# Performance work log

Hardware: AMD Instinct MI355X
Metric: run time of the kernel (lower is better)

The kernel has to match this reference:

```python
import jax, jax.numpy as jnp
import numpy as np

B, L, IN_DIM, H, KD = 2, 2048, 1024, 16, 64
SCALE = float(np.sqrt(IN_DIM / H))  # sqrt(in_dim / num_heads), per ScaledDotAttention
LN_EPS = 1e-5


def setup_inputs() -> dict:
    key = jax.random.key(0)
    ks = jax.random.split(key, 12)
    s_in = 1.0 / np.sqrt(IN_DIM)
    s_hd = 1.0 / np.sqrt(H * KD)
    return {
        "q": jax.random.normal(ks[0], (B, L, IN_DIM), jnp.float32),
        "k": jax.random.normal(ks[1], (B, L, IN_DIM), jnp.float32),
        "v": jax.random.normal(ks[2], (B, L, IN_DIM), jnp.float32),
        "Wq": jax.random.normal(ks[3], (IN_DIM, H * KD), jnp.float32) * s_in,
        "bq": jnp.zeros((H * KD,), jnp.float32),
        "Wk": jax.random.normal(ks[4], (IN_DIM, H * KD), jnp.float32) * s_in,
        "bk": jnp.zeros((H * KD,), jnp.float32),
        "Wv": jax.random.normal(ks[5], (IN_DIM, H * KD), jnp.float32) * s_in,
        "bv": jnp.zeros((H * KD,), jnp.float32),
        "Wo": jax.random.normal(ks[6], (H * KD, IN_DIM), jnp.float32) * s_hd,
        "bo": jnp.zeros((IN_DIM,), jnp.float32),
        "gamma": jnp.ones((IN_DIM,), jnp.float32),
        "beta": jnp.zeros((IN_DIM,), jnp.float32),
    }


def _split_heads(x):
    # [B, L, H*KD] -> [H*B, L, KD]  (heads MAJOR, matching permute(2,0,1,3).view)
    b, l, _ = x.shape
    return x.reshape(b, l, H, KD).transpose(2, 0, 1, 3).reshape(H * b, l, KD)


def reference(q, k, v, Wq, bq, Wk, bk, Wv, bv, Wo, bo, gamma, beta):
    res = q
    qh = _split_heads(q @ Wq + bq)   # [H*B, Lq, KD]
    kh = _split_heads(k @ Wk + bk)
    vh = _split_heads(v @ Wv + bv)
    scores = jnp.einsum("zqd,zkd->zqk", qh, kh) / SCALE
    atn = jax.nn.softmax(scores, axis=-1)          # [H*B, Lq, Lk]
    out = jnp.einsum("zqk,zkd->zqd", atn, vh)      # [H*B, Lq, KD]
    b = q.shape[0]
    out = out.reshape(H, b, -1, KD).transpose(1, 2, 0, 3).reshape(b, -1, H * KD)
    out = out @ Wo + bo
    x = out + res
    mu = jnp.mean(x, axis=-1, keepdims=True)
    var = jnp.mean(jnp.square(x - mu), axis=-1, keepdims=True)
    out = (x - mu) * jax.lax.rsqrt(var + LN_EPS) * gamma + beta
    return (out, atn)
```

## Files before the change

kernel.cpp:

```cpp
#include <hip/hip_runtime.h>
#include <hip/hip_bf16.h>

typedef unsigned short u16;
typedef unsigned int   u32;

using bf16x8 = __attribute__((ext_vector_type(8))) short;
using f32x4  = __attribute__((ext_vector_type(4))) float;

#define SEQ  2048
#define NZ   32
#define KTOT 1024
#define NTOT 1024
#define SC2  0.18033688011112042f

__device__ __forceinline__ u16 f2bf(float f) {
    union { float f; u32 u; } x; x.f = f;
    u32 r = x.u + 0x7fffu + ((x.u >> 16) & 1u);
    return (u16)(r >> 16);
}

__device__ __forceinline__ void gl_lds16(const u16* g, u16* ldsbase) {
    __builtin_amdgcn_global_load_lds(
        (const __attribute__((address_space(1))) u32*)g,
        (__attribute__((address_space(3))) u32*)ldsbase, 16, 0, 0);
}

__global__ __launch_bounds__(256) void prep_k(const float* __restrict__ q,
                                              const float* __restrict__ k,
                                              const float* __restrict__ v,
                                              const float* __restrict__ W0,
                                              const float* __restrict__ W1,
                                              const float* __restrict__ W2,
                                              const float* __restrict__ W3,
                                              u16* __restrict__ qb,
                                              u16* __restrict__ WT) {
    __shared__ u16 t[64 * 65];
    const int tid = threadIdx.x;
    const int b = blockIdx.x;
    if (b < 6144) {
        const int zc = b >> 11;
        const int xc = b & 2047;
        const float* src = (zc == 0) ? q : (zc == 1) ? k : v;
        u16* dst = qb + (size_t)zc * 4096 * 1024;
        int off = xc * 2048 + tid * 8;
        float4 v0 = *(const float4*)&src[off];
        float4 v1 = *(const float4*)&src[off + 4];
        uint4 o;
        o.x = (u32)f2bf(v0.x) | ((u32)f2bf(v0.y) << 16);
        o.y = (u32)f2bf(v0.z) | ((u32)f2bf(v0.w) << 16);
        o.z = (u32)f2bf(v1.x) | ((u32)f2bf(v1.y) << 16);
        o.w = (u32)f2bf(v1.z) | ((u32)f2bf(v1.w) << 16);
        *(uint4*)&dst[off] = o;
        return;
    }
    const int tt = b - 6144;
    const int zz = tt >> 8;
    const int bx = tt & 15, by = (tt >> 4) & 15;
    const float* W = (zz == 0) ? W0 : (zz == 1) ? W1 : (zz == 2) ? W2 : W3;
    u16* out = WT + (size_t)zz * 1024 * 1024;
    const int n0 = bx * 64, k0 = by * 64;
#pragma unroll
    for (int it = 0; it < 4; ++it) {
        int flat = it * 256 + tid;
        int r = flat >> 4, c4 = (flat & 15) * 4;
        float4 vv = *(const float4*)&W[(k0 + r) * 1024 + n0 + c4];
        t[r * 65 + c4 + 0] = f2bf(vv.x);
        t[r * 65 + c4 + 1] = f2bf(vv.y);
        t[r * 65 + c4 + 2] = f2bf(vv.z);
        t[r * 65 + c4 + 3] = f2bf(vv.w);
    }
    __syncthreads();
#pragma unroll
    for (int it = 0; it < 2; ++it) {
        int flat = it * 256 + tid;
        int rn = flat >> 3, c8 = (flat & 7) * 8;
        u32 p[4];
#pragma unroll
        for (int e = 0; e < 4; ++e) {
            u32 lo = t[(c8 + 2 * e + 0) * 65 + rn];
            u32 hi = t[(c8 + 2 * e + 1) * 65 + rn];
            p[e] = lo | (hi << 16);
        }
        uint4 o; o.x = p[0]; o.y = p[1]; o.z = p[2]; o.w = p[3];
        *(uint4*)&out[(n0 + rn) * 1024 + k0 + c8] = o;
    }
}

__global__ __launch_bounds__(256) void qkvproj_k(const u16* __restrict__ qb,
                                                 const u16* __restrict__ wt,
                                                 const float* __restrict__ bq,
                                                 const float* __restrict__ bk,
                                                 const float* __restrict__ bv,
                                                 u16* __restrict__ qh,
                                                 u16* __restrict__ kh,
                                                 u16* __restrict__ vhT) {
    __shared__ u16 As[128 * 32];
    __shared__ u16 Bs[128 * 32];
    __shared__ u16 T[128 * 132];
    const int zz = blockIdx.z;
    const u16*   A    = qb + (size_t)zz * 4096 * 1024;
    const u16*   WT   = wt + (size_t)zz * 1024 * 1024;
    const float* bias = (zz == 0) ? bq : (zz == 1) ? bk : bv;
    const bool vmode = (zz == 2);

    const int tid = threadIdx.x;
    const int m0 = blockIdx.y * 128;
    const int n0 = blockIdx.x * 128;
    const int wid = tid >> 6, lane = tid & 63;
    const int wrow = wid >> 1, wcol = wid & 1;
    const int g = lane >> 4, li = lane & 15;

    f32x4 acc[4][4];
#pragma unroll
    for (int a = 0; a < 4; ++a)
#pragma unroll
        for (int b = 0; b < 4; ++b) acc[a][b] = (f32x4){0.f, 0.f, 0.f, 0.f};

    for (int kt = 0; kt < KTOT / 32; ++kt) {
        const int kb = kt * 32;
#pragma unroll
        for (int cc = 0; cc < 2; ++cc) {
            int c = wid + cc * 4;
            gl_lds16(&A[(m0 + c * 16 + (lane >> 2)) * KTOT + kb + (lane & 3) * 8],
                     &As[c * 512]);
            gl_lds16(&WT[(n0 + c * 16 + (lane >> 2)) * KTOT + kb + (lane & 3) * 8],
                     &Bs[c * 512]);
        }
        __syncthreads();
        bf16x8 af[4], bfr[4];
#pragma unroll
        for (int fr = 0; fr < 4; ++fr)
            af[fr] = *(const bf16x8*)&As[(wrow * 64 + fr * 16 + li) * 32 + g * 8];
#pragma unroll
        for (int fc = 0; fc < 4; ++fc)
            bfr[fc] = *(const bf16x8*)&Bs[(wcol * 64 + fc * 16 + li) * 32 + g * 8];
#pragma unroll
        for (int fr = 0; fr < 4; ++fr)
#pragma unroll
            for (int fc = 0; fc < 4; ++fc)
                acc[fr][fc] = __builtin_amdgcn_mfma_f32_16x16x32_bf16(
                    af[fr], bfr[fc], acc[fr][fc], 0, 0, 0);
        __syncthreads();
    }

#pragma unroll
    for (int fr = 0; fr < 4; ++fr)
#pragma unroll
        for (int fc = 0; fc < 4; ++fc)
#pragma unroll
            for (int reg = 0; reg < 4; ++reg) {
                int rl = wrow * 64 + fr * 16 + g * 4 + reg;
                int cl = wcol * 64 + fc * 16 + li;
                u16 bv16 = f2bf(acc[fr][fc][reg] + bias[n0 + cl]);
                if (!vmode) T[rl * 132 + cl] = bv16;
                else        T[cl * 132 + rl] = bv16;
            }
    __syncthreads();

    const int bb2 = m0 >> 11, ml = m0 & 2047;
    const int lc8 = (tid & 7) * 8;
#pragma unroll
    for (int it = 0; it < 8; ++it) {
        int idx = it * 32 + (tid >> 3);
        int row = idx >> 1, half = idx & 1;
        uint4 val = *(const uint4*)&T[row * 132 + half * 64 + lc8];
        if (!vmode) {
            int h = (n0 >> 6) + half;
            u16* dst = (blockIdx.z == 0) ? qh : kh;
            *(uint4*)&dst[(((h * 2 + bb2) * 2048 + ml + row) << 6) + lc8] = val;
        } else {
            int cg = n0 + row;
            int h = cg >> 6, d = cg & 63;
            *(uint4*)&vhT[(((h * 2 + bb2) * 64 + d) << 11) + ml + half * 64 + lc8] = val;
        }
    }
}

__global__ __launch_bounds__(256) void outproj_k(const u16* __restrict__ A,
                                                 const u16* __restrict__ WT,
                                                 const float* __restrict__ bias,
                                                 const float* __restrict__ res,
                                                 float* __restrict__ outp) {
    __shared__ u16 As[64 * 32];
    __shared__ u16 Bs[128 * 32];
    const int tid = threadIdx.x;
    const int m0 = blockIdx.y * 64;
    const int n0 = blockIdx.x * 128;
    const int wid = tid >> 6, lane = tid & 63;
    const int wrow = wid >> 1, wcol = wid & 1;
    const int g = lane >> 4, li = lane & 15;

    f32x4 acc[2][4];
#pragma unroll
    for (int a = 0; a < 2; ++a)
#pragma unroll
        for (int b = 0; b < 4; ++b) acc[a][b] = (f32x4){0.f, 0.f, 0.f, 0.f};

    for (int kt = 0; kt < KTOT / 32; ++kt) {
        const int kb = kt * 32;
        gl_lds16(&A[(m0 + wid * 16 + (lane >> 2)) * KTOT + kb + (lane & 3) * 8],
                 &As[wid * 512]);
#pragma unroll
        for (int cc = 0; cc < 2; ++cc) {
            int c = wid * 2 + cc;
            gl_lds16(&WT[(n0 + c * 16 + (lane >> 2)) * KTOT + kb + (lane & 3) * 8],
                     &Bs[c * 512]);
        }
        __syncthreads();
        bf16x8 af[2], bfr[4];
#pragma unroll
        for (int fr = 0; fr < 2; ++fr)
            af[fr] = *(const bf16x8*)&As[(wrow * 32 + fr * 16 + li) * 32 + g * 8];
#pragma unroll
        for (int fc = 0; fc < 4; ++fc)
            bfr[fc] = *(const bf16x8*)&Bs[(wcol * 64 + fc * 16 + li) * 32 + g * 8];
#pragma unroll
        for (int fr = 0; fr < 2; ++fr)
#pragma unroll
            for (int fc = 0; fc < 4; ++fc)
                acc[fr][fc] = __builtin_amdgcn_mfma_f32_16x16x32_bf16(
                    af[fr], bfr[fc], acc[fr][fc], 0, 0, 0);
        __syncthreads();
    }

#pragma unroll
    for (int fr = 0; fr < 2; ++fr)
#pragma unroll
        for (int fc = 0; fc < 4; ++fc)
#pragma unroll
            for (int reg = 0; reg < 4; ++reg) {
                int r = m0 + wrow * 32 + fr * 16 + g * 4 + reg;
                int c = n0 + wcol * 64 + fc * 16 + li;
                outp[r * NTOT + c] = acc[fr][fc][reg] + bias[c] + res[r * NTOT + c];
            }
}

__global__ __launch_bounds__(256, 4) void attn_k(const u16* __restrict__ qh,
                                                 const u16* __restrict__ kh,
                                                 const u16* __restrict__ vhT,
                                                 float* __restrict__ atn,
                                                 u16* __restrict__ attnout) {
    __shared__ u16 lds[20480];
    const int tid = threadIdx.x;
    const int D = blockIdx.x;
    const int z = D & 31, q0 = (D >> 5) * 64;
    const int h = z >> 1, bb = z & 1;
    const int wid = tid >> 6, lane = tid & 63, g = lane >> 4, li = lane & 15;
    const int row0 = wid * 16;
    const int zbase = z * SEQ;
    const int swz = li & 7;

    bf16x8 aq[2];
#pragma unroll
    for (int ks = 0; ks < 2; ++ks)
        aq[ks] = *(const bf16x8*)
            &qh[(size_t)(zbase + q0 + row0 + li) * 64 + ks * 32 + g * 8];

    float lmv;
    {
        u16* KsA = lds;
        const int ar = lane >> 3;
        const int ac = (lane & 7) ^ ar;
        const u16* kA[4];
#pragma unroll
        for (int cc = 0; cc < 4; ++cc) {
            int c = wid * 4 + cc;
            kA[cc] = &kh[(size_t)(zbase + c * 8 + ar) * 64 + ac * 8];
            gl_lds16(kA[cc], &KsA[c * 512]);
        }
        __syncthreads();

        float s = 0.f;
        for (int kt = 0; kt < 16; ++kt) {
            const int buf = kt & 1;
            if (kt < 15) {
                const size_t nxt = (size_t)(kt + 1) * 128 * 64;
#pragma unroll
                for (int cc = 0; cc < 4; ++cc)
                    gl_lds16(kA[cc] + nxt,
                             &KsA[(buf ^ 1) * 8192 + (wid * 4 + cc) * 512]);
            }
            f32x4 sv[8];
#pragma unroll
            for (int fc = 0; fc < 8; ++fc) sv[fc] = (f32x4){0.f, 0.f, 0.f, 0.f};
            __builtin_amdgcn_s_setprio(1);
#pragma unroll
            for (int ks = 0; ks < 2; ++ks) {
#pragma unroll
                for (int fc = 0; fc < 8; ++fc) {
                    bf16x8 kf = *(const bf16x8*)
                        &KsA[buf * 8192 + (fc * 16 + li) * 64 + (((ks * 4 + g) ^ swz) * 8)];
                    sv[fc] = __builtin_amdgcn_mfma_f32_16x16x32_bf16(
                        kf, aq[ks], sv[fc], 0, 0, 0);
                }
            }
            __builtin_amdgcn_s_setprio(0);
            float ssum = 0.f;
#pragma unroll
            for (int fc = 0; fc < 8; ++fc)
#pragma unroll
                for (int reg = 0; reg < 4; ++reg)
                    ssum += __builtin_amdgcn_exp2f(sv[fc][reg] * SC2);
            s += ssum;
            __syncthreads();
        }
        s += __shfl_xor(s, 16, 64);
        s += __shfl_xor(s, 32, 64);
        lmv = __builtin_amdgcn_logf(s);
    }

    u16* Ks = lds;
    u16* Vs = lds + 8192;
    u16* Ps = lds + 16384;
    const int ar8 = lane >> 3;
    const int schunk = (lane & 7) ^ ar8;
    const u16* ksrc[2];
    const u16* vsrc[2];
#pragma unroll
    for (int cc = 0; cc < 2; ++cc) {
        int c = wid * 2 + cc;
        ksrc[cc] = &kh[(size_t)(zbase + c * 8 + ar8) * 64 + schunk * 8];
        vsrc[cc] = &vhT[(size_t)(z * 64 + c * 8 + ar8) * SEQ + schunk * 8];
        gl_lds16(ksrc[cc], &Ks[c * 512]);
        gl_lds16(vsrc[cc], &Vs[c * 512]);
    }
    __syncthreads();

    f32x4 oa[4];
#pragma unroll
    for (int fn = 0; fn < 4; ++fn) oa[fn] = (f32x4){0.f, 0.f, 0.f, 0.f};

    const u16* psw = &Ps[wid * 1024];
    const int prow = wid * 1024 + li * 64;
    for (int kt = 0; kt < 32; ++kt) {
        const int buf = kt & 1;
        const int k0 = kt * 64;
        if (kt < 31) {
#pragma unroll
            for (int cc = 0; cc < 2; ++cc) {
                int c = wid * 2 + cc;
                gl_lds16(ksrc[cc] + (size_t)(kt + 1) * 64 * 64,
                         &Ks[(buf ^ 1) * 4096 + c * 512]);
                gl_lds16(vsrc[cc] + (size_t)(kt + 1) * 64,
                         &Vs[(buf ^ 1) * 4096 + c * 512]);
            }
        }

        f32x4 sv[4];
#pragma unroll
        for (int fc = 0; fc < 4; ++fc) sv[fc] = (f32x4){0.f, 0.f, 0.f, 0.f};
        __builtin_amdgcn_s_setprio(1);
#pragma unroll
        for (int ks = 0; ks < 2; ++ks) {
#pragma unroll
            for (int fc = 0; fc < 4; ++fc) {
                bf16x8 kf = *(const bf16x8*)
                    &Ks[buf * 4096 + (fc * 16 + li) * 64 + (((ks * 4 + g) ^ swz) * 8)];
                sv[fc] = __builtin_amdgcn_mfma_f32_16x16x32_bf16(
                    kf, aq[ks], sv[fc], 0, 0, 0);
            }
        }
        __builtin_amdgcn_s_setprio(0);

#pragma unroll
        for (int fc = 0; fc < 4; ++fc) {
            float p0 = __builtin_amdgcn_exp2f(sv[fc][0] * SC2 - lmv);
            float p1 = __builtin_amdgcn_exp2f(sv[fc][1] * SC2 - lmv);
            float p2 = __builtin_amdgcn_exp2f(sv[fc][2] * SC2 - lmv);
            float p3 = __builtin_amdgcn_exp2f(sv[fc][3] * SC2 - lmv);
            u32 w0 = (u32)f2bf(p0) | ((u32)f2bf(p1) << 16);
            u32 w1 = (u32)f2bf(p2) | ((u32)f2bf(p3) << 16);
            int pc = ((fc * 2 + (g >> 1)) ^ swz) * 8 + (g & 1) * 4;
            *(u32*)&Ps[prow + pc]     = w0;
            *(u32*)&Ps[prow + pc + 2] = w1;
        }

#pragma unroll
        for (int it2 = 0; it2 < 4; ++it2) {
            int row  = it2 * 4 + (lane >> 4);
            int col8 = lane & 15;
            int lc   = col8 >> 1;
            uint2 d2 = *(const uint2*)
                &psw[row * 64 + ((lc ^ (row & 7)) << 3) + ((col8 & 1) << 2)];
            f32x4 o4;
            union { u32 u; float f; } c0v, c1v, c2v, c3v;
            c0v.u = (d2.x & 0xffffu) << 16;  c1v.u = d2.x & 0xffff0000u;
            c2v.u = (d2.y & 0xffffu) << 16;  c3v.u = d2.y & 0xffff0000u;
            o4[0] = c0v.f; o4[1] = c1v.f; o4[2] = c2v.f; o4[3] = c3v.f;
            __builtin_nontemporal_store(o4, (f32x4*)
                &atn[(size_t)(zbase + q0 + row0 + row) * SEQ + k0 + col8 * 4]);
        }

        __builtin_amdgcn_s_setprio(1);
#pragma unroll
        for (int ks = 0; ks < 2; ++ks) {
            bf16x8 pf = *(const bf16x8*)&Ps[prow + (((ks * 4 + g) ^ swz) * 8)];
#pragma unroll
            for (int fn = 0; fn < 4; ++fn) {
                bf16x8 vf = *(const bf16x8*)
                    &Vs[buf * 4096 + (fn * 16 + li) * 64 + (((ks * 4 + g) ^ swz) * 8)];
                oa[fn] = __builtin_amdgcn_mfma_f32_16x16x32_bf16(
                    vf, pf, oa[fn], 0, 0, 0);
            }
        }
        __builtin_amdgcn_s_setprio(0);
        asm volatile("s_waitcnt vmcnt(4) lgkmcnt(0)" ::: "memory");
        __builtin_amdgcn_s_barrier();
    }

#pragma unroll
    for (int fn = 0; fn < 4; ++fn) {
        u32 w0 = (u32)f2bf(oa[fn][0]) | ((u32)f2bf(oa[fn][1]) << 16);
        u32 w1 = (u32)f2bf(oa[fn][2]) | ((u32)f2bf(oa[fn][3]) << 16);
        uint2 wv; wv.x = w0; wv.y = w1;
        *(uint2*)&attnout[(size_t)(bb * SEQ + q0 + row0 + li) * 1024
                          + h * 64 + fn * 16 + g * 4] = wv;
    }
}

__global__ __launch_bounds__(256) void ln_k(const float* __restrict__ y,
                                            const float* __restrict__ gamma,
                                            const float* __restrict__ beta,
                                            float* __restrict__ out) {
    __shared__ float red[8];
    const int row = blockIdx.x, tid = threadIdx.x;
    float4 v = *(const float4*)&y[row * 1024 + tid * 4];
    float s = v.x + v.y + v.z + v.w;
    float sq = v.x * v.x + v.y * v.y + v.z * v.z + v.w * v.w;
#pragma unroll
    for (int msk = 1; msk <= 32; msk <<= 1) {
        s += __shfl_xor(s, msk, 64);
        sq += __shfl_xor(sq, msk, 64);
    }
    const int wid = tid >> 6;
    if ((tid & 63) == 0) { red[wid * 2] = s; red[wid * 2 + 1] = sq; }
    __syncthreads();
    s = red[0] + red[2] + red[4] + red[6];
    sq = red[1] + red[3] + red[5] + red[7];
    float mu = s * (1.0f / 1024.0f);
    float var = sq * (1.0f / 1024.0f) - mu * mu;
    float rs = rsqrtf(var + 1e-5f);
    float4 g4 = *(const float4*)&gamma[tid * 4];
    float4 b4 = *(const float4*)&beta[tid * 4];
    float4 o;
    o.x = (v.x - mu) * rs * g4.x + b4.x;
    o.y = (v.y - mu) * rs * g4.y + b4.y;
    o.z = (v.z - mu) * rs * g4.z + b4.z;
    o.w = (v.w - mu) * rs * g4.w + b4.w;
    *(float4*)&out[row * 1024 + tid * 4] = o;
}

extern "C" void kernel_launch(void* const* d_in, const int* in_sizes, int n_in,
                              void* d_out, int out_size, void* d_ws, size_t ws_size,
                              hipStream_t stream) {
    const float* q     = (const float*)d_in[0];
    const float* k     = (const float*)d_in[1];
    const float* v     = (const float*)d_in[2];
    const float* Wq    = (const float*)d_in[3];
    const float* bq    = (const float*)d_in[4];
    const float* Wk    = (const float*)d_in[5];
    const float* bk    = (const float*)d_in[6];
    const float* Wv    = (const float*)d_in[7];
    const float* bv    = (const float*)d_in[8];
    const float* Wo    = (const float*)d_in[9];
    const float* bo    = (const float*)d_in[10];
    const float* gamma = (const float*)d_in[11];
    const float* beta  = (const float*)d_in[12];

    float* out = (float*)d_out;
    float* atn = out + 4096 * 1024;

    u16* wt  = (u16*)d_ws;
    u16* qb  = wt + 4 * 1024 * 1024;
    u16* attnout = qb;
    float* y = (float*)(qb + 4096 * 1024);
    u16* qh  = qb + 3 * 4096 * 1024;
    u16* kh  = qh + NZ * SEQ * 64;
    u16* vhT = kh + NZ * SEQ * 64;
    u16* wto = wt + 3 * 1024 * 1024;

    dim3 tb(256);
    prep_k<<<dim3(7168), tb, 0, stream>>>(q, k, v, Wq, Wk, Wv, Wo, qb, wt);

    qkvproj_k<<<dim3(8, 32, 3), tb, 0, stream>>>(qb, wt, bq, bk, bv,
                                                 qh, kh, vhT);

    attn_k<<<dim3(1024), dim3(256), 0, stream>>>(qh, kh, vhT, atn, attnout);

    outproj_k<<<dim3(8, 64), tb, 0, stream>>>(attnout, wto, bo, q, y);

    ln_k<<<dim3(4096), tb, 0, stream>>>(y, gamma, beta, out);
}
```

Baseline: 244.4 us.

## Process two 16-row query sets per wave in attention to reuse K/V tiles

Each attention block now covers 128 query rows instead of 64, with every wave computing two 16-row sets that share each K and V fragment read from LDS. This halves the grid and the K/V global-to-LDS traffic per query row, and amortises LDS fragment reads across twice the MFMA work. The cost is more registers and LDS per block, lower occupancy (launch bound from 4 to 3), only 512 blocks across the CUs, and a retuned vmcnt wait for the larger number of outstanding stores. The attention-matrix stores, which likely dominate this kernel, are unchanged in volume.

```diff
diff --git a/kernel.cpp b/kernel.cpp
--- a/kernel.cpp
+++ b/kernel.cpp
@@ -235,28 +235,31 @@
             }
 }
 
-__global__ __launch_bounds__(256, 4) void attn_k(const u16* __restrict__ qh,
+__global__ __launch_bounds__(256, 3) void attn_k(const u16* __restrict__ qh,
                                                  const u16* __restrict__ kh,
                                                  const u16* __restrict__ vhT,
                                                  float* __restrict__ atn,
                                                  u16* __restrict__ attnout) {
-    __shared__ u16 lds[20480];
+    __shared__ u16 lds[24576];
     const int tid = threadIdx.x;
     const int D = blockIdx.x;
-    const int z = D & 31, q0 = (D >> 5) * 64;
+    const int z = D & 31, q0 = (D >> 5) * 128;
     const int h = z >> 1, bb = z & 1;
     const int wid = tid >> 6, lane = tid & 63, g = lane >> 4, li = lane & 15;
-    const int row0 = wid * 16;
+    const int row0 = wid * 32;
     const int zbase = z * SEQ;
     const int swz = li & 7;
 
-    bf16x8 aq[2];
-#pragma unroll
-    for (int ks = 0; ks < 2; ++ks)
-        aq[ks] = *(const bf16x8*)
-            &qh[(size_t)(zbase + q0 + row0 + li) * 64 + ks * 32 + g * 8];
-
-    float lmv;
+    bf16x8 aq[2][2];
+#pragma unroll
+    for (int set = 0; set < 2; ++set)
+#pragma unroll
+        for (int ks = 0; ks < 2; ++ks)
+            aq[set][ks] = *(const bf16x8*)
+                &qh[(size_t)(zbase + q0 + row0 + set * 16 + li) * 64
+                    + ks * 32 + g * 8];
+
+    float lmv0, lmv1;
     {
         u16* KsA = lds;
         const int ar = lane >> 3;
@@ -270,7 +273,7 @@
         }
         __syncthreads();
 
-        float s = 0.f;
+        float s0 = 0.f, s1 = 0.f;
         for (int kt = 0; kt < 16; ++kt) {
             const int buf = kt & 1;
             if (kt < 15) {
@@ -280,9 +283,12 @@
                     gl_lds16(kA[cc] + nxt,
                              &KsA[(buf ^ 1) * 8192 + (wid * 4 + cc) * 512]);
             }
-            f32x4 sv[8];
-#pragma unroll
-            for (int fc = 0; fc < 8; ++fc) sv[fc] = (f32x4){0.f, 0.f, 0.f, 0.f};
+            f32x4 sv0[8], sv1[8];
+#pragma unroll
+            for (int fc = 0; fc < 8; ++fc) {
+                sv0[fc] = (f32x4){0.f, 0.f, 0.f, 0.f};
+                sv1[fc] = (f32x4){0.f, 0.f, 0.f, 0.f};
+            }
             __builtin_amdgcn_s_setprio(1);
 #pragma unroll
             for (int ks = 0; ks < 2; ++ks) {
@@ -290,23 +296,30 @@
                 for (int fc = 0; fc < 8; ++fc) {
                     bf16x8 kf = *(const bf16x8*)
                         &KsA[buf * 8192 + (fc * 16 + li) * 64 + (((ks * 4 + g) ^ swz) * 8)];
-                    sv[fc] = __builtin_amdgcn_mfma_f32_16x16x32_bf16(
-                        kf, aq[ks], sv[fc], 0, 0, 0);
+                    sv0[fc] = __builtin_amdgcn_mfma_f32_16x16x32_bf16(
+                        kf, aq[0][ks], sv0[fc], 0, 0, 0);
+                    sv1[fc] = __builtin_amdgcn_mfma_f32_16x16x32_bf16(
+                        kf, aq[1][ks], sv1[fc], 0, 0, 0);
                 }
             }
             __builtin_amdgcn_s_setprio(0);
-            float ssum = 0.f;
+            float a0 = 0.f, a1 = 0.f;
 #pragma unroll
             for (int fc = 0; fc < 8; ++fc)
 #pragma unroll
-                for (int reg = 0; reg < 4; ++reg)
-                    ssum += __builtin_amdgcn_exp2f(sv[fc][reg] * SC2);
-            s += ssum;
+                for (int reg = 0; reg < 4; ++reg) {
+                    a0 += __builtin_amdgcn_exp2f(sv0[fc][reg] * SC2);
+                    a1 += __builtin_amdgcn_exp2f(sv1[fc][reg] * SC2);
+                }
+            s0 += a0; s1 += a1;
             __syncthreads();
         }
-        s += __shfl_xor(s, 16, 64);
-        s += __shfl_xor(s, 32, 64);
-        lmv = __builtin_amdgcn_logf(s);
+        s0 += __shfl_xor(s0, 16, 64);
+        s0 += __shfl_xor(s0, 32, 64);
+        s1 += __shfl_xor(s1, 16, 64);
+        s1 += __shfl_xor(s1, 32, 64);
+        lmv0 = __builtin_amdgcn_logf(s0);
+        lmv1 = __builtin_amdgcn_logf(s1);
     }
 
     u16* Ks = lds;
@@ -326,12 +339,15 @@
     }
     __syncthreads();
 
-    f32x4 oa[4];
-#pragma unroll
-    for (int fn = 0; fn < 4; ++fn) oa[fn] = (f32x4){0.f, 0.f, 0.f, 0.f};
-
-    const u16* psw = &Ps[wid * 1024];
-    const int prow = wid * 1024 + li * 64;
+    f32x4 oa[2][4];
+#pragma unroll
+    for (int set = 0; set < 2; ++set)
+#pragma unroll
+        for (int fn = 0; fn < 4; ++fn) oa[set][fn] = (f32x4){0.f, 0.f, 0.f, 0.f};
+
+    const int pswb  = wid * 2048;
+    const int prow0 = pswb + li * 64;
+    const int prow1 = prow0 + 1024;
     for (int kt = 0; kt < 32; ++kt) {
         const int buf = kt & 1;
         const int k0 = kt * 64;
@@ -346,9 +362,12 @@
             }
         }
 
-        f32x4 sv[4];
-#pragma unroll
-        for (int fc = 0; fc < 4; ++fc) sv[fc] = (f32x4){0.f, 0.f, 0.f, 0.f};
+        f32x4 sv0[4], sv1[4];
+#pragma unroll
+        for (int fc = 0; fc < 4; ++fc) {
+            sv0[fc] = (f32x4){0.f, 0.f, 0.f, 0.f};
+            sv1[fc] = (f32x4){0.f, 0.f, 0.f, 0.f};
+        }
         __builtin_amdgcn_s_setprio(1);
 #pragma unroll
         for (int ks = 0; ks < 2; ++ks) {
@@ -356,66 +375,90 @@
             for (int fc = 0; fc < 4; ++fc) {
                 bf16x8 kf = *(const bf16x8*)
                     &Ks[buf * 4096 + (fc * 16 + li) * 64 + (((ks * 4 + g) ^ swz) * 8)];
-                sv[fc] = __builtin_amdgcn_mfma_f32_16x16x32_bf16(
-                    kf, aq[ks], sv[fc], 0, 0, 0);
+                sv0[fc] = __builtin_amdgcn_mfma_f32_16x16x32_bf16(
+                    kf, aq[0][ks], sv0[fc], 0, 0, 0);
+                sv1[fc] = __builtin_amdgcn_mfma_f32_16x16x32_bf16(
+                    kf, aq[1][ks], sv1[fc], 0, 0, 0);
             }
         }
         __builtin_amdgcn_s_setprio(0);
 
 #pragma unroll
         for (int fc = 0; fc < 4; ++fc) {
-            float p0 = __builtin_amdgcn_exp2f(sv[fc][0] * SC2 - lmv);
-            float p1 = __builtin_amdgcn_exp2f(sv[fc][1] * SC2 - lmv);
-            float p2 = __builtin_amdgcn_exp2f(sv[fc][2] * SC2 - lmv);
-            float p3 = __builtin_amdgcn_exp2f(sv[fc][3] * SC2 - lmv);
-            u32 w0 = (u32)f2bf(p0) | ((u32)f2bf(p1) << 16);
-            u32 w1 = (u32)f2bf(p2) | ((u32)f2bf(p3) << 16);
+            float p0 = __builtin_amdgcn_exp2f(sv0[fc][0] * SC2 - lmv0);
+            float p1 = __builtin_amdgcn_exp2f(sv0[fc][1] * SC2 - lmv0);
+            float p2 = __builtin_amdgcn_exp2f(sv0[fc][2] * SC2 - lmv0);
+            float p3 = __builtin_amdgcn_exp2f(sv0[fc][3] * SC2 - lmv0);
+            uint2 wv;
+            wv.x = (u32)f2bf(p0) | ((u32)f2bf(p1) << 16);
+            wv.y = (u32)f2bf(p2) | ((u32)f2bf(p3) << 16);
             int pc = ((fc * 2 + (g >> 1)) ^ swz) * 8 + (g & 1) * 4;
-            *(u32*)&Ps[prow + pc]     = w0;
-            *(u32*)&Ps[prow + pc + 2] = w1;
-        }
-
-#pragma unroll
-        for (int it2 = 0; it2 < 4; ++it2) {
-            int row  = it2 * 4 + (lane >> 4);
-            int col8 = lane & 15;
-            int lc   = col8 >> 1;
-            uint2 d2 = *(const uint2*)
-                &psw[row * 64 + ((lc ^ (row & 7)) << 3) + ((col8 & 1) << 2)];
-            f32x4 o4;
-            union { u32 u; float f; } c0v, c1v, c2v, c3v;
-            c0v.u = (d2.x & 0xffffu) << 16;  c1v.u = d2.x & 0xffff0000u;
-            c2v.u = (d2.y & 0xffffu) << 16;  c3v.u = d2.y & 0xffff0000u;
-            o4[0] = c0v.f; o4[1] = c1v.f; o4[2] = c2v.f; o4[3] = c3v.f;
-            __builtin_nontemporal_store(o4, (f32x4*)
-                &atn[(size_t)(zbase + q0 + row0 + row) * SEQ + k0 + col8 * 4]);
+            *(uint2*)&Ps[prow0 + pc] = wv;
+        }
+#pragma unroll
+        for (int fc = 0; fc < 4; ++fc) {
+            float p0 = __builtin_amdgcn_exp2f(sv1[fc][0] * SC2 - lmv1);
+            float p1 = __builtin_amdgcn_exp2f(sv1[fc][1] * SC2 - lmv1);
+            float p2 = __builtin_amdgcn_exp2f(sv1[fc][2] * SC2 - lmv1);
+            float p3 = __builtin_amdgcn_exp2f(sv1[fc][3] * SC2 - lmv1);
+            uint2 wv;
+            wv.x = (u32)f2bf(p0) | ((u32)f2bf(p1) << 16);
+            wv.y = (u32)f2bf(p2) | ((u32)f2bf(p3) << 16);
+            int pc = ((fc * 2 + (g >> 1)) ^ swz) * 8 + (g & 1) * 4;
+            *(uint2*)&Ps[prow1 + pc] = wv;
+        }
+
+#pragma unroll
+        for (int set = 0; set < 2; ++set) {
+#pragma unroll
+            for (int it2 = 0; it2 < 4; ++it2) {
+                int row  = it2 * 4 + (lane >> 4);
+                int col8 = lane & 15;
+                int lc   = col8 >> 1;
+                uint2 d2 = *(const uint2*)
+                    &Ps[pswb + set * 1024 + row * 64
+                        + ((lc ^ (row & 7)) << 3) + ((col8 & 1) << 2)];
+                f32x4 o4;
+                union { u32 u; float f; } c0v, c1v, c2v, c3v;
+                c0v.u = (d2.x & 0xffffu) << 16;  c1v.u = d2.x & 0xffff0000u;
+                c2v.u = (d2.y & 0xffffu) << 16;  c3v.u = d2.y & 0xffff0000u;
+                o4[0] = c0v.f; o4[1] = c1v.f; o4[2] = c2v.f; o4[3] = c3v.f;
+                __builtin_nontemporal_store(o4, (f32x4*)
+                    &atn[(size_t)(zbase + q0 + row0 + set * 16 + row) * SEQ
+                         + k0 + col8 * 4]);
+            }
         }
 
         __builtin_amdgcn_s_setprio(1);
 #pragma unroll
         for (int ks = 0; ks < 2; ++ks) {
-            bf16x8 pf = *(const bf16x8*)&Ps[prow + (((ks * 4 + g) ^ swz) * 8)];
+            bf16x8 pf0 = *(const bf16x8*)&Ps[prow0 + (((ks * 4 + g) ^ swz) * 8)];
+            bf16x8 pf1 = *(const bf16x8*)&Ps[prow1 + (((ks * 4 + g) ^ swz) * 8)];
 #pragma unroll
             for (int fn = 0; fn < 4; ++fn) {
                 bf16x8 vf = *(const bf16x8*)
                     &Vs[buf * 4096 + (fn * 16 + li) * 64 + (((ks * 4 + g) ^ swz) * 8)];
-                oa[fn] = __builtin_amdgcn_mfma_f32_16x16x32_bf16(
-                    vf, pf, oa[fn], 0, 0, 0);
+                oa[0][fn] = __builtin_amdgcn_mfma_f32_16x16x32_bf16(
+                    vf, pf0, oa[0][fn], 0, 0, 0);
+                oa[1][fn] = __builtin_amdgcn_mfma_f32_16x16x32_bf16(
+                    vf, pf1, oa[1][fn], 0, 0, 0);
             }
         }
         __builtin_amdgcn_s_setprio(0);
-        asm volatile("s_waitcnt vmcnt(4) lgkmcnt(0)" ::: "memory");
+        asm volatile("s_waitcnt vmcnt(8) lgkmcnt(0)" ::: "memory");
         __builtin_amdgcn_s_barrier();
     }
 
 #pragma unroll
-    for (int fn = 0; fn < 4; ++fn) {
-        u32 w0 = (u32)f2bf(oa[fn][0]) | ((u32)f2bf(oa[fn][1]) << 16);
-        u32 w1 = (u32)f2bf(oa[fn][2]) | ((u32)f2bf(oa[fn][3]) << 16);
-        uint2 wv; wv.x = w0; wv.y = w1;
-        *(uint2*)&attnout[(size_t)(bb * SEQ + q0 + row0 + li) * 1024
-                          + h * 64 + fn * 16 + g * 4] = wv;
-    }
+    for (int set = 0; set < 2; ++set)
+#pragma unroll
+        for (int fn = 0; fn < 4; ++fn) {
+            u32 w0 = (u32)f2bf(oa[set][fn][0]) | ((u32)f2bf(oa[set][fn][1]) << 16);
+            u32 w1 = (u32)f2bf(oa[set][fn][2]) | ((u32)f2bf(oa[set][fn][3]) << 16);
+            uint2 wv; wv.x = w0; wv.y = w1;
+            *(uint2*)&attnout[(size_t)(bb * SEQ + q0 + row0 + set * 16 + li) * 1024
+                              + h * 64 + fn * 16 + g * 4] = wv;
+        }
 }
 
 __global__ __launch_bounds__(256) void ln_k(const float* __restrict__ y,
@@ -485,7 +528,7 @@
     qkvproj_k<<<dim3(8, 32, 3), tb, 0, stream>>>(qb, wt, bq, bk, bv,
                                                  qh, kh, vhT);
 
-    attn_k<<<dim3(1024), dim3(256), 0, stream>>>(qh, kh, vhT, atn, attnout);
+    attn_k<<<dim3(512), dim3(256), 0, stream>>>(qh, kh, vhT, atn, attnout);
 
     outproj_k<<<dim3(8, 64), tb, 0, stream>>>(attnout, wto, bo, q, y);
 
```

After: 250.2 us. 2.3% more time.
